# Kernel tuning notes

Hardware: AMD Instinct MI355X
Metric: run time of the kernel (lower is better)

The kernel has to match this reference:

```python
import jax, jax.numpy as jnp
import numpy as np

DIM = 1024
NUM_HEADS = 16
HEAD_DIM = DIM // NUM_HEADS
SCALE = HEAD_DIM ** (-0.5)
B, N = 2, 2048


def setup_inputs() -> dict:
    key = jax.random.key(0)
    ks = jax.random.split(key, 9)
    s = DIM ** (-0.5)
    return {
        "x": jax.random.normal(ks[0], (B, N, DIM), dtype=jnp.float32),
        "Wq": jax.random.normal(ks[1], (DIM, DIM), dtype=jnp.float32) * s,
        "bq": jax.random.normal(ks[2], (DIM,), dtype=jnp.float32) * 0.01,
        "Wk": jax.random.normal(ks[3], (DIM, DIM), dtype=jnp.float32) * s,
        "bk": jax.random.normal(ks[4], (DIM,), dtype=jnp.float32) * 0.01,
        "Wv": jax.random.normal(ks[5], (DIM, DIM), dtype=jnp.float32) * s,
        "bv": jax.random.normal(ks[6], (DIM,), dtype=jnp.float32) * 0.01,
        "Wp": jax.random.normal(ks[7], (DIM, DIM), dtype=jnp.float32) * s,
        "bp": jax.random.normal(ks[8], (DIM,), dtype=jnp.float32) * 0.01,
    }


def reference(x, Wq, bq, Wk, bk, Wv, bv, Wp, bp):
    Bb, Nn, C = x.shape
    # Linear layers (torch Linear: x @ W.T + b)
    q = x @ Wq.T + bq
    k = x @ Wk.T + bk
    v = x @ Wv.T + bv
    # [B, H, N, Dh]
    q = q.reshape(Bb, Nn, NUM_HEADS, HEAD_DIM).transpose(0, 2, 1, 3) * SCALE
    k = k.reshape(Bb, Nn, NUM_HEADS, HEAD_DIM).transpose(0, 2, 1, 3)
    v = v.reshape(Bb, Nn, NUM_HEADS, HEAD_DIM).transpose(0, 2, 1, 3)
    # float32 scores (original casts q,k to float before matmul)
    attn = jnp.einsum("bhnd,bhmd->bhnm", q.astype(jnp.float32), k.astype(jnp.float32))
    attn = jax.nn.softmax(attn, axis=-1).astype(x.dtype)
    out = jnp.einsum("bhnm,bhmd->bhnd", attn, v)
    out = out.transpose(0, 2, 1, 3).reshape(Bb, Nn, C)
    return out @ Wp.T + bp
```

## Files before the change

kernel.cpp:

```cpp
#include <hip/hip_runtime.h>
#include <hip/hip_bf16.h>
#include <stdint.h>

#define SEQ   2048
#define NDIM  1024
#define NH    16
#define DH    64
#define NB    2
#define MROWS (NB*SEQ)
#define ATTN_SCALE 0.125f

typedef __attribute__((ext_vector_type(8))) short bf16x8;
typedef __attribute__((ext_vector_type(4))) float f32x4;


__device__ __forceinline__ unsigned short f2bf(float f) {
  union { float f; unsigned int u; } v; v.f = f;
  unsigned int u = v.u;
  return (unsigned short)((u + 0x7fffu + ((u >> 16) & 1u)) >> 16);
}

__device__ __forceinline__ void gld16(const void* g, void* l) {
  __builtin_amdgcn_global_load_lds(
      (const __attribute__((address_space(1))) void*)g,
      (__attribute__((address_space(3))) void*)l,
      16, 0, 0);
}

__global__ __launch_bounds__(256) void cvt_all(
    const float* __restrict__ x,  const float* __restrict__ wq,
    const float* __restrict__ wk, const float* __restrict__ wv,
    const float* __restrict__ wp,
    unsigned short* __restrict__ xb,  unsigned short* __restrict__ wqb,
    unsigned short* __restrict__ wkb, unsigned short* __restrict__ wvb,
    unsigned short* __restrict__ wpb)
{
  int c = blockIdx.x * 256 + threadIdx.x;
  const float* s; unsigned short* d;
  if (c < (MROWS*NDIM/8)) { s = x; d = xb; }
  else {
    c -= MROWS*NDIM/8;
    int w = c >> 17; c &= (1<<17)-1;
    s = (w==0)?wq:(w==1)?wk:(w==2)?wv:wp;
    d = (w==0)?wqb:(w==1)?wkb:(w==2)?wvb:wpb;
  }
  size_t off = (size_t)c * 8;
  const float4* sp = (const float4*)(s + off);
  float4 a = sp[0], b4 = sp[1];
  unsigned int u0 = (unsigned)f2bf(a.x)  | ((unsigned)f2bf(a.y)  << 16);
  unsigned int u1 = (unsigned)f2bf(a.z)  | ((unsigned)f2bf(a.w)  << 16);
  unsigned int u2 = (unsigned)f2bf(b4.x) | ((unsigned)f2bf(b4.y) << 16);
  unsigned int u3 = (unsigned)f2bf(b4.z) | ((unsigned)f2bf(b4.w) << 16);
  uint4 o; o.x = u0; o.y = u1; o.z = u2; o.w = u3;
  *(uint4*)(d + off) = o;
}

__device__ __forceinline__ void gemm128_loop(
    const unsigned short* __restrict__ A0,
    const unsigned short* __restrict__ B0,
    int K, f32x4 acc[4][4], char* ldsA, char* ldsB)
{
  const int tid = threadIdx.x;
  const int lane = tid & 63;
  const int g    = lane >> 4;
  const int l15  = lane & 15;
  const int wv   = tid >> 6;
  const int wm   = wv >> 1;
  const int wn   = wv & 1;

  int srow[2], scol[2];
#pragma unroll
  for (int p = 0; p < 2; ++p) {
    int idx = p*256 + tid;
    int row = idx >> 2, cpos = idx & 3;
    srow[p] = row;
    scol[p] = (cpos ^ ((row >> 1) & 3)) * 8;
  }
  int offA[4], offB[4];
#pragma unroll
  for (int f = 0; f < 4; ++f) {
    int ra = wm*64 + f*16 + l15;
    offA[f] = ra*64 + ((g ^ ((ra >> 1) & 3)) * 16);
    int rb = wn*64 + f*16 + l15;
    offB[f] = rb*64 + ((g ^ ((rb >> 1) & 3)) * 16);
  }

  for (int k0 = 0; k0 < K; k0 += 32) {
#pragma unroll
    for (int p = 0; p < 2; ++p) {
      gld16(A0 + (size_t)srow[p]*K + k0 + scol[p], ldsA + p*4096 + wv*1024);
      gld16(B0 + (size_t)srow[p]*K + k0 + scol[p], ldsB + p*4096 + wv*1024);
    }
    __syncthreads();
    bf16x8 af[4], bfr[4];
#pragma unroll
    for (int f = 0; f < 4; ++f) {
      af[f]  = *(const bf16x8*)(ldsA + offA[f]);
      bfr[f] = *(const bf16x8*)(ldsB + offB[f]);
    }
#pragma unroll
    for (int i = 0; i < 4; ++i)
#pragma unroll
      for (int j = 0; j < 4; ++j)
        acc[i][j] = __builtin_amdgcn_mfma_f32_16x16x32_bf16(af[i], bfr[j], acc[i][j], 0, 0, 0);
    __syncthreads();
  }
}

__global__ __launch_bounds__(256, 3) void gemm_qkv(
    const unsigned short* __restrict__ xb,
    const unsigned short* __restrict__ wqb, const unsigned short* __restrict__ wkb,
    const unsigned short* __restrict__ wvb,
    const float* __restrict__ bq, const float* __restrict__ bk, const float* __restrict__ bv,
    unsigned short* __restrict__ qb, unsigned short* __restrict__ kb,
    unsigned short* __restrict__ vtb)
{
  __shared__ __align__(16) char lds[16384];
  const int z = blockIdx.z;
  const unsigned short* W = (z==0)?wqb:(z==1)?wkb:wvb;
  const float* bias = (z==0)?bq:(z==1)?bk:bv;
  const int n0 = blockIdx.x * 128, m0 = blockIdx.y * 128;

  f32x4 acc[4][4];
#pragma unroll
  for (int i = 0; i < 4; ++i)
#pragma unroll
    for (int j = 0; j < 4; ++j) acc[i][j] = (f32x4){0.f, 0.f, 0.f, 0.f};

  gemm128_loop(xb + (size_t)m0*NDIM, W + (size_t)n0*NDIM, NDIM, acc, lds, lds + 8192);

  const int lane = threadIdx.x & 63, g = lane >> 4, l15 = lane & 15;
  const int wvx = threadIdx.x >> 6, wm = wvx >> 1, wn = wvx & 1;

  if (z < 2) {
    unsigned short* out = (z==0) ? qb : kb;
#pragma unroll
    for (int i = 0; i < 4; ++i)
#pragma unroll
      for (int j = 0; j < 4; ++j) {
        int col = n0 + wn*64 + j*16 + l15;
        float bb = bias[col];
#pragma unroll
        for (int r = 0; r < 4; ++r) {
          int row = m0 + wm*64 + i*16 + g*4 + r;
          out[(size_t)row*NDIM + col] = f2bf(acc[i][j][r] + bb);
        }
      }
  } else {
#pragma unroll
    for (int i = 0; i < 4; ++i)
#pragma unroll
      for (int j = 0; j < 4; ++j) {
        int col = n0 + wn*64 + j*16 + l15;
        float bb = bias[col];
        int row0 = m0 + wm*64 + i*16 + g*4;
        int b_ = row0 >> 11, n_ = row0 & (SEQ-1);
        unsigned long long pk =
            (unsigned long long)f2bf(acc[i][j][0] + bb)
          | ((unsigned long long)f2bf(acc[i][j][1] + bb) << 16)
          | ((unsigned long long)f2bf(acc[i][j][2] + bb) << 32)
          | ((unsigned long long)f2bf(acc[i][j][3] + bb) << 48);
        *(unsigned long long*)(vtb + ((size_t)(b_*NDIM + col))*SEQ + n_) = pk;
      }
  }
}

__global__ __launch_bounds__(256, 2) void attn_fwd(
    const unsigned short* __restrict__ qb, const unsigned short* __restrict__ kb,
    const unsigned short* __restrict__ vtb, unsigned short* __restrict__ ob)
{
  __shared__ __align__(16) char lds[32768];
  char* Ks = lds;
  char* Vs = lds + 8192;
  const int tid = threadIdx.x, lane = tid & 63, g = lane >> 4, l15 = lane & 15;
  const int wvx = tid >> 6;
  char* Pw = lds + 16384 + wvx*4096;
  const int bh = blockIdx.y, b_ = bh >> 4, h = bh & 15;
  const int qbase = blockIdx.x*128 + wvx*32;

  bf16x8 qf[2][2];
#pragma unroll
  for (int fn = 0; fn < 2; ++fn)
#pragma unroll
    for (int kc = 0; kc < 2; ++kc) {
      size_t row = (size_t)(b_*SEQ + qbase + fn*16 + l15);
      qf[fn][kc] = *(const bf16x8*)(qb + row*NDIM + h*DH + kc*32 + g*8);
    }

  float m_[2] = {-3.0e38f, -3.0e38f};
  float l_[2] = {0.f, 0.f};
  f32x4 o_[2][4];
#pragma unroll
  for (int fn = 0; fn < 2; ++fn)
#pragma unroll
    for (int fd = 0; fd < 4; ++fd) o_[fn][fd] = (f32x4){0.f, 0.f, 0.f, 0.f};

  for (int t = 0; t < SEQ/64; ++t) {
    const int k0t = t*64;
#pragma unroll
    for (int p = 0; p < 2; ++p) {
      int idx = p*256 + tid;
      int row = idx >> 3, cpos = idx & 7;
      int gc8 = (cpos ^ (row & 7)) * 8;
      gld16(kb  + ((size_t)(b_*SEQ + k0t + row))*NDIM + h*DH + gc8,
            Ks + p*4096 + wvx*1024);
      gld16(vtb + ((size_t)(b_*NDIM + h*DH + row))*SEQ + k0t + gc8,
            Vs + p*4096 + wvx*1024);
    }
    __syncthreads();

    bf16x8 kf[4][2];
#pragma unroll
    for (int fm = 0; fm < 4; ++fm)
#pragma unroll
      for (int kc = 0; kc < 2; ++kc) {
        int row = fm*16 + l15;
        kf[fm][kc] = *(const bf16x8*)(Ks + row*128 + (((kc*4+g) ^ (row & 7))*16));
      }

    f32x4 st[2][4];
#pragma unroll
    for (int fn = 0; fn < 2; ++fn)
#pragma unroll
      for (int fm = 0; fm < 4; ++fm) st[fn][fm] = (f32x4){0.f, 0.f, 0.f, 0.f};
#pragma unroll
    for (int kc = 0; kc < 2; ++kc)
#pragma unroll
      for (int fn = 0; fn < 2; ++fn)
#pragma unroll
        for (int fm = 0; fm < 4; ++fm)
          st[fn][fm] = __builtin_amdgcn_mfma_f32_16x16x32_bf16(kf[fm][kc], qf[fn][kc], st[fn][fm], 0, 0, 0);

#pragma unroll
    for (int fn = 0; fn < 2; ++fn) {
      float xs[4][4];
      float tmax = -3.0e38f;
#pragma unroll
      for (int fm = 0; fm < 4; ++fm)
#pragma unroll
        for (int r = 0; r < 4; ++r) {
          float v = st[fn][fm][r] * ATTN_SCALE;
          xs[fm][r] = v;
          tmax = fmaxf(tmax, v);
        }
      tmax = fmaxf(tmax, __shfl_xor(tmax, 16));
      tmax = fmaxf(tmax, __shfl_xor(tmax, 32));
      float mnew  = fmaxf(m_[fn], tmax);
      float alpha = __expf(m_[fn] - mnew);
      m_[fn] = mnew;
      float rsum = 0.f;
      const int prow = fn*16 + l15;
#pragma unroll
      for (int fm = 0; fm < 4; ++fm) {
        float p0 = __expf(xs[fm][0] - mnew);
        float p1 = __expf(xs[fm][1] - mnew);
        float p2 = __expf(xs[fm][2] - mnew);
        float p3 = __expf(xs[fm][3] - mnew);
        rsum += (p0 + p1) + (p2 + p3);
        unsigned long long pk =
            (unsigned long long)f2bf(p0)
          | ((unsigned long long)f2bf(p1) << 16)
          | ((unsigned long long)f2bf(p2) << 32)
          | ((unsigned long long)f2bf(p3) << 48);
        *(unsigned long long*)(Pw + prow*128 + (((fm*2 + (g>>1)) ^ (prow & 7))*16) + (g & 1)*8) = pk;
      }
      rsum += __shfl_xor(rsum, 16);
      rsum += __shfl_xor(rsum, 32);
      l_[fn] = l_[fn]*alpha + rsum;
#pragma unroll
      for (int fd = 0; fd < 4; ++fd)
#pragma unroll
        for (int r = 0; r < 4; ++r) o_[fn][fd][r] *= alpha;
    }

    bf16x8 vf[4][2];
#pragma unroll
    for (int fd = 0; fd < 4; ++fd)
#pragma unroll
      for (int ks = 0; ks < 2; ++ks) {
        int row = fd*16 + l15;
        vf[fd][ks] = *(const bf16x8*)(Vs + row*128 + (((ks*4+g) ^ (row & 7))*16));
      }
    bf16x8 pf[2][2];
#pragma unroll
    for (int fn = 0; fn < 2; ++fn)
#pragma unroll
      for (int ks = 0; ks < 2; ++ks) {
        int row = fn*16 + l15;
        pf[fn][ks] = *(const bf16x8*)(Pw + row*128 + (((ks*4+g) ^ (row & 7))*16));
      }
#pragma unroll
    for (int ks = 0; ks < 2; ++ks)
#pragma unroll
      for (int fn = 0; fn < 2; ++fn)
#pragma unroll
        for (int fd = 0; fd < 4; ++fd)
          o_[fn][fd] = __builtin_amdgcn_mfma_f32_16x16x32_bf16(vf[fd][ks], pf[fn][ks], o_[fn][fd], 0, 0, 0);

    __syncthreads();
  }

#pragma unroll
  for (int fn = 0; fn < 2; ++fn) {
    float inv = 1.f / l_[fn];
    size_t row = (size_t)(b_*SEQ + qbase + fn*16 + l15);
#pragma unroll
    for (int fd = 0; fd < 4; ++fd) {
      unsigned long long pk =
          (unsigned long long)f2bf(o_[fn][fd][0]*inv)
        | ((unsigned long long)f2bf(o_[fn][fd][1]*inv) << 16)
        | ((unsigned long long)f2bf(o_[fn][fd][2]*inv) << 32)
        | ((unsigned long long)f2bf(o_[fn][fd][3]*inv) << 48);
      *(unsigned long long*)(ob + row*NDIM + h*DH + fd*16 + g*4) = pk;
    }
  }
}

__global__ __launch_bounds__(256, 3) void gemm_proj(
    const unsigned short* __restrict__ ob, const unsigned short* __restrict__ wpb,
    const float* __restrict__ bp, float* __restrict__ out)
{
  __shared__ __align__(16) char lds[16384];
  const int n0 = blockIdx.x * 128, m0 = blockIdx.y * 128;
  f32x4 acc[4][4];
#pragma unroll
  for (int i = 0; i < 4; ++i)
#pragma unroll
    for (int j = 0; j < 4; ++j) acc[i][j] = (f32x4){0.f, 0.f, 0.f, 0.f};

  gemm128_loop(ob + (size_t)m0*NDIM, wpb + (size_t)n0*NDIM, NDIM, acc, lds, lds + 8192);

  const int lane = threadIdx.x & 63, g = lane >> 4, l15 = lane & 15;
  const int wvx = threadIdx.x >> 6, wm = wvx >> 1, wn = wvx & 1;
#pragma unroll
  for (int i = 0; i < 4; ++i)
#pragma unroll
    for (int j = 0; j < 4; ++j) {
      int col = n0 + wn*64 + j*16 + l15;
      float bb = bp[col];
#pragma unroll
      for (int r = 0; r < 4; ++r) {
        int row = m0 + wm*64 + i*16 + g*4 + r;
        out[(size_t)row*NDIM + col] = acc[i][j][r] + bb;
      }
    }
}

extern "C" void kernel_launch(void* const* d_in, const int* in_sizes, int n_in,
                              void* d_out, int out_size, void* d_ws, size_t ws_size,
                              hipStream_t stream) {
  const float* x  = (const float*)d_in[0];
  const float* Wq = (const float*)d_in[1];
  const float* bq = (const float*)d_in[2];
  const float* Wk = (const float*)d_in[3];
  const float* bk = (const float*)d_in[4];
  const float* Wv = (const float*)d_in[5];
  const float* bv = (const float*)d_in[6];
  const float* Wp = (const float*)d_in[7];
  const float* bp = (const float*)d_in[8];
  float* out = (float*)d_out;

  char* ws = (char*)d_ws;
  const size_t MB = (size_t)1 << 20;
  unsigned short* xb  = (unsigned short*)(ws + 0*MB);
  unsigned short* wqb = (unsigned short*)(ws + 8*MB);
  unsigned short* wkb = (unsigned short*)(ws + 10*MB);
  unsigned short* wvb = (unsigned short*)(ws + 12*MB);
  unsigned short* wpb = (unsigned short*)(ws + 14*MB);
  unsigned short* qb  = (unsigned short*)(ws + 16*MB);
  unsigned short* kb  = (unsigned short*)(ws + 24*MB);
  unsigned short* vtb = (unsigned short*)(ws + 32*MB);
  unsigned short* ob  = (unsigned short*)(ws + 40*MB);

  hipLaunchKernelGGL(cvt_all, dim3(4096), dim3(256), 0, stream,
                     x, Wq, Wk, Wv, Wp, xb, wqb, wkb, wvb, wpb);
  hipLaunchKernelGGL(gemm_qkv, dim3(NDIM/128, MROWS/128, 3), dim3(256), 0, stream,
                     xb, wqb, wkb, wvb, bq, bk, bv, qb, kb, vtb);
  hipLaunchKernelGGL(attn_fwd, dim3(SEQ/128, NB*NH), dim3(256), 0, stream,
                     qb, kb, vtb, ob);
  hipLaunchKernelGGL(gemm_proj, dim3(NDIM/128, MROWS/128), dim3(256), 0, stream,
                     ob, wpb, bp, out);
}
```

Measured before the change: 216.0 us.

## Shrink attention and projection tiles for more blocks, use exp2 softmax with lazy rescale

The attention kernel now handles 64 query rows per block (16 per wave) instead of 128, with less LDS and a higher launch bound, which doubles the grid to fill more CUs. Softmax folds log2(e) into the scale, uses the hardware exp2 instruction, and skips the rescale of the accumulators when no row max increases. The output projection GEMM is templated to use 64-row M tiles, doubling its block count. In exchange, each K/V tile loaded into LDS is reused by fewer query rows, so K/V load traffic per output row goes up.

```diff
diff --git a/kernel.cpp b/kernel.cpp
--- a/kernel.cpp
+++ b/kernel.cpp
@@ -9,6 +9,7 @@
 #define NB    2
 #define MROWS (NB*SEQ)
 #define ATTN_SCALE 0.125f
+#define S2SCALE (0.125f * 1.44269504f)
 
 typedef __attribute__((ext_vector_type(8))) short bf16x8;
 typedef __attribute__((ext_vector_type(4))) float f32x4;
@@ -18,6 +19,14 @@
   union { float f; unsigned int u; } v; v.f = f;
   unsigned int u = v.u;
   return (unsigned short)((u + 0x7fffu + ((u >> 16) & 1u)) >> 16);
+}
+
+__device__ __forceinline__ float exp2fast(float x) {
+#if __has_builtin(__builtin_amdgcn_exp2f)
+  return __builtin_amdgcn_exp2f(x);
+#else
+  float r; asm volatile("v_exp_f32 %0, %1" : "=v"(r) : "v"(x)); return r;
+#endif
 }
 
 __device__ __forceinline__ void gld16(const void* g, void* l) {
@@ -55,11 +64,14 @@
   *(uint4*)(d + off) = o;
 }
 
-__device__ __forceinline__ void gemm128_loop(
+template<int BM>
+__device__ __forceinline__ void gemm_loop(
     const unsigned short* __restrict__ A0,
     const unsigned short* __restrict__ B0,
-    int K, f32x4 acc[4][4], char* ldsA, char* ldsB)
-{
+    int K, f32x4 (&acc)[BM/32][4], char* ldsA, char* ldsB)
+{
+  constexpr int MI = BM/32;
+  constexpr int AP = BM/64;
   const int tid = threadIdx.x;
   const int lane = tid & 63;
   const int g    = lane >> 4;
@@ -68,38 +80,48 @@
   const int wm   = wv >> 1;
   const int wn   = wv & 1;
 
-  int srow[2], scol[2];
+  int srowA[AP], scolA[AP], srowB[2], scolB[2];
+#pragma unroll
+  for (int p = 0; p < AP; ++p) {
+    int idx = p*256 + tid;
+    int row = idx >> 2, cpos = idx & 3;
+    srowA[p] = row;
+    scolA[p] = (cpos ^ ((row >> 1) & 3)) * 8;
+  }
 #pragma unroll
   for (int p = 0; p < 2; ++p) {
     int idx = p*256 + tid;
     int row = idx >> 2, cpos = idx & 3;
-    srow[p] = row;
-    scol[p] = (cpos ^ ((row >> 1) & 3)) * 8;
-  }
-  int offA[4], offB[4];
+    srowB[p] = row;
+    scolB[p] = (cpos ^ ((row >> 1) & 3)) * 8;
+  }
+  int offA[MI], offB[4];
+#pragma unroll
+  for (int f = 0; f < MI; ++f) {
+    int ra = wm*(BM/2) + f*16 + l15;
+    offA[f] = ra*64 + ((g ^ ((ra >> 1) & 3)) * 16);
+  }
 #pragma unroll
   for (int f = 0; f < 4; ++f) {
-    int ra = wm*64 + f*16 + l15;
-    offA[f] = ra*64 + ((g ^ ((ra >> 1) & 3)) * 16);
     int rb = wn*64 + f*16 + l15;
     offB[f] = rb*64 + ((g ^ ((rb >> 1) & 3)) * 16);
   }
 
   for (int k0 = 0; k0 < K; k0 += 32) {
 #pragma unroll
-    for (int p = 0; p < 2; ++p) {
-      gld16(A0 + (size_t)srow[p]*K + k0 + scol[p], ldsA + p*4096 + wv*1024);
-      gld16(B0 + (size_t)srow[p]*K + k0 + scol[p], ldsB + p*4096 + wv*1024);
-    }
+    for (int p = 0; p < AP; ++p)
+      gld16(A0 + (size_t)srowA[p]*K + k0 + scolA[p], ldsA + p*4096 + wv*1024);
+#pragma unroll
+    for (int p = 0; p < 2; ++p)
+      gld16(B0 + (size_t)srowB[p]*K + k0 + scolB[p], ldsB + p*4096 + wv*1024);
     __syncthreads();
-    bf16x8 af[4], bfr[4];
-#pragma unroll
-    for (int f = 0; f < 4; ++f) {
-      af[f]  = *(const bf16x8*)(ldsA + offA[f]);
-      bfr[f] = *(const bf16x8*)(ldsB + offB[f]);
-    }
-#pragma unroll
-    for (int i = 0; i < 4; ++i)
+    bf16x8 af[MI], bfr[4];
+#pragma unroll
+    for (int f = 0; f < MI; ++f) af[f] = *(const bf16x8*)(ldsA + offA[f]);
+#pragma unroll
+    for (int f = 0; f < 4;  ++f) bfr[f] = *(const bf16x8*)(ldsB + offB[f]);
+#pragma unroll
+    for (int i = 0; i < MI; ++i)
 #pragma unroll
       for (int j = 0; j < 4; ++j)
         acc[i][j] = __builtin_amdgcn_mfma_f32_16x16x32_bf16(af[i], bfr[j], acc[i][j], 0, 0, 0);
@@ -127,7 +149,7 @@
 #pragma unroll
     for (int j = 0; j < 4; ++j) acc[i][j] = (f32x4){0.f, 0.f, 0.f, 0.f};
 
-  gemm128_loop(xb + (size_t)m0*NDIM, W + (size_t)n0*NDIM, NDIM, acc, lds, lds + 8192);
+  gemm_loop<128>(xb + (size_t)m0*NDIM, W + (size_t)n0*NDIM, NDIM, acc, lds, lds + 8192);
 
   const int lane = threadIdx.x & 63, g = lane >> 4, l15 = lane & 15;
   const int wvx = threadIdx.x >> 6, wm = wvx >> 1, wn = wvx & 1;
@@ -165,35 +187,32 @@
   }
 }
 
-__global__ __launch_bounds__(256, 2) void attn_fwd(
+__global__ __launch_bounds__(256, 4) void attn_fwd(
     const unsigned short* __restrict__ qb, const unsigned short* __restrict__ kb,
     const unsigned short* __restrict__ vtb, unsigned short* __restrict__ ob)
 {
-  __shared__ __align__(16) char lds[32768];
+  __shared__ __align__(16) char lds[24576];
   char* Ks = lds;
   char* Vs = lds + 8192;
   const int tid = threadIdx.x, lane = tid & 63, g = lane >> 4, l15 = lane & 15;
   const int wvx = tid >> 6;
-  char* Pw = lds + 16384 + wvx*4096;
+  char* Pw = lds + 16384 + wvx*2048;
   const int bh = blockIdx.y, b_ = bh >> 4, h = bh & 15;
-  const int qbase = blockIdx.x*128 + wvx*32;
-
-  bf16x8 qf[2][2];
-#pragma unroll
-  for (int fn = 0; fn < 2; ++fn)
-#pragma unroll
-    for (int kc = 0; kc < 2; ++kc) {
-      size_t row = (size_t)(b_*SEQ + qbase + fn*16 + l15);
-      qf[fn][kc] = *(const bf16x8*)(qb + row*NDIM + h*DH + kc*32 + g*8);
-    }
-
-  float m_[2] = {-3.0e38f, -3.0e38f};
-  float l_[2] = {0.f, 0.f};
-  f32x4 o_[2][4];
-#pragma unroll
-  for (int fn = 0; fn < 2; ++fn)
-#pragma unroll
-    for (int fd = 0; fd < 4; ++fd) o_[fn][fd] = (f32x4){0.f, 0.f, 0.f, 0.f};
+  const int qbase = blockIdx.x*64 + wvx*16;
+
+  bf16x8 qf[2];
+  {
+    size_t row = (size_t)(b_*SEQ + qbase + l15);
+#pragma unroll
+    for (int kc = 0; kc < 2; ++kc)
+      qf[kc] = *(const bf16x8*)(qb + row*NDIM + h*DH + kc*32 + g*8);
+  }
+
+  float m2 = -3.0e38f;
+  float l_ = 0.f;
+  f32x4 o_[4];
+#pragma unroll
+  for (int fd = 0; fd < 4; ++fd) o_[fd] = (f32x4){0.f, 0.f, 0.f, 0.f};
 
   for (int t = 0; t < SEQ/64; ++t) {
     const int k0t = t*64;
@@ -218,60 +237,55 @@
         kf[fm][kc] = *(const bf16x8*)(Ks + row*128 + (((kc*4+g) ^ (row & 7))*16));
       }
 
-    f32x4 st[2][4];
-#pragma unroll
-    for (int fn = 0; fn < 2; ++fn)
-#pragma unroll
-      for (int fm = 0; fm < 4; ++fm) st[fn][fm] = (f32x4){0.f, 0.f, 0.f, 0.f};
+    f32x4 st[4];
+#pragma unroll
+    for (int fm = 0; fm < 4; ++fm) st[fm] = (f32x4){0.f, 0.f, 0.f, 0.f};
 #pragma unroll
     for (int kc = 0; kc < 2; ++kc)
 #pragma unroll
-      for (int fn = 0; fn < 2; ++fn)
-#pragma unroll
-        for (int fm = 0; fm < 4; ++fm)
-          st[fn][fm] = __builtin_amdgcn_mfma_f32_16x16x32_bf16(kf[fm][kc], qf[fn][kc], st[fn][fm], 0, 0, 0);
-
-#pragma unroll
-    for (int fn = 0; fn < 2; ++fn) {
-      float xs[4][4];
-      float tmax = -3.0e38f;
-#pragma unroll
       for (int fm = 0; fm < 4; ++fm)
-#pragma unroll
-        for (int r = 0; r < 4; ++r) {
-          float v = st[fn][fm][r] * ATTN_SCALE;
-          xs[fm][r] = v;
-          tmax = fmaxf(tmax, v);
-        }
-      tmax = fmaxf(tmax, __shfl_xor(tmax, 16));
-      tmax = fmaxf(tmax, __shfl_xor(tmax, 32));
-      float mnew  = fmaxf(m_[fn], tmax);
-      float alpha = __expf(m_[fn] - mnew);
-      m_[fn] = mnew;
-      float rsum = 0.f;
-      const int prow = fn*16 + l15;
-#pragma unroll
-      for (int fm = 0; fm < 4; ++fm) {
-        float p0 = __expf(xs[fm][0] - mnew);
-        float p1 = __expf(xs[fm][1] - mnew);
-        float p2 = __expf(xs[fm][2] - mnew);
-        float p3 = __expf(xs[fm][3] - mnew);
-        rsum += (p0 + p1) + (p2 + p3);
-        unsigned long long pk =
-            (unsigned long long)f2bf(p0)
-          | ((unsigned long long)f2bf(p1) << 16)
-          | ((unsigned long long)f2bf(p2) << 32)
-          | ((unsigned long long)f2bf(p3) << 48);
-        *(unsigned long long*)(Pw + prow*128 + (((fm*2 + (g>>1)) ^ (prow & 7))*16) + (g & 1)*8) = pk;
-      }
-      rsum += __shfl_xor(rsum, 16);
-      rsum += __shfl_xor(rsum, 32);
-      l_[fn] = l_[fn]*alpha + rsum;
+        st[fm] = __builtin_amdgcn_mfma_f32_16x16x32_bf16(kf[fm][kc], qf[kc], st[fm], 0, 0, 0);
+
+    float xs[4][4];
+    float tmax = -3.0e38f;
+#pragma unroll
+    for (int fm = 0; fm < 4; ++fm)
+#pragma unroll
+      for (int r = 0; r < 4; ++r) {
+        float v = st[fm][r] * S2SCALE;
+        xs[fm][r] = v;
+        tmax = fmaxf(tmax, v);
+      }
+    tmax = fmaxf(tmax, __shfl_xor(tmax, 16));
+    tmax = fmaxf(tmax, __shfl_xor(tmax, 32));
+    if (__any(tmax > m2)) {
+      float mnew  = fmaxf(m2, tmax);
+      float alpha = exp2fast(m2 - mnew);
+      m2 = mnew;
+      l_ *= alpha;
 #pragma unroll
       for (int fd = 0; fd < 4; ++fd)
 #pragma unroll
-        for (int r = 0; r < 4; ++r) o_[fn][fd][r] *= alpha;
-    }
+        for (int r = 0; r < 4; ++r) o_[fd][r] *= alpha;
+    }
+    float rsum = 0.f;
+#pragma unroll
+    for (int fm = 0; fm < 4; ++fm) {
+      float p0 = exp2fast(xs[fm][0] - m2);
+      float p1 = exp2fast(xs[fm][1] - m2);
+      float p2 = exp2fast(xs[fm][2] - m2);
+      float p3 = exp2fast(xs[fm][3] - m2);
+      rsum += (p0 + p1) + (p2 + p3);
+      unsigned long long pk =
+          (unsigned long long)f2bf(p0)
+        | ((unsigned long long)f2bf(p1) << 16)
+        | ((unsigned long long)f2bf(p2) << 32)
+        | ((unsigned long long)f2bf(p3) << 48);
+      *(unsigned long long*)(Pw + l15*128 + (((fm*2 + (g>>1)) ^ (l15 & 7))*16) + (g & 1)*8) = pk;
+    }
+    rsum += __shfl_xor(rsum, 16);
+    rsum += __shfl_xor(rsum, 32);
+    l_ += rsum;
 
     bf16x8 vf[4][2];
 #pragma unroll
@@ -281,66 +295,59 @@
         int row = fd*16 + l15;
         vf[fd][ks] = *(const bf16x8*)(Vs + row*128 + (((ks*4+g) ^ (row & 7))*16));
       }
-    bf16x8 pf[2][2];
-#pragma unroll
-    for (int fn = 0; fn < 2; ++fn)
-#pragma unroll
-      for (int ks = 0; ks < 2; ++ks) {
-        int row = fn*16 + l15;
-        pf[fn][ks] = *(const bf16x8*)(Pw + row*128 + (((ks*4+g) ^ (row & 7))*16));
-      }
+    bf16x8 pf[2];
 #pragma unroll
     for (int ks = 0; ks < 2; ++ks)
-#pragma unroll
-      for (int fn = 0; fn < 2; ++fn)
-#pragma unroll
-        for (int fd = 0; fd < 4; ++fd)
-          o_[fn][fd] = __builtin_amdgcn_mfma_f32_16x16x32_bf16(vf[fd][ks], pf[fn][ks], o_[fn][fd], 0, 0, 0);
+      pf[ks] = *(const bf16x8*)(Pw + l15*128 + (((ks*4+g) ^ (l15 & 7))*16));
+#pragma unroll
+    for (int ks = 0; ks < 2; ++ks)
+#pragma unroll
+      for (int fd = 0; fd < 4; ++fd)
+        o_[fd] = __builtin_amdgcn_mfma_f32_16x16x32_bf16(vf[fd][ks], pf[ks], o_[fd], 0, 0, 0);
 
     __syncthreads();
   }
 
-#pragma unroll
-  for (int fn = 0; fn < 2; ++fn) {
-    float inv = 1.f / l_[fn];
-    size_t row = (size_t)(b_*SEQ + qbase + fn*16 + l15);
+  {
+    float inv = 1.f / l_;
+    size_t row = (size_t)(b_*SEQ + qbase + l15);
 #pragma unroll
     for (int fd = 0; fd < 4; ++fd) {
       unsigned long long pk =
-          (unsigned long long)f2bf(o_[fn][fd][0]*inv)
-        | ((unsigned long long)f2bf(o_[fn][fd][1]*inv) << 16)
-        | ((unsigned long long)f2bf(o_[fn][fd][2]*inv) << 32)
-        | ((unsigned long long)f2bf(o_[fn][fd][3]*inv) << 48);
+          (unsigned long long)f2bf(o_[fd][0]*inv)
+        | ((unsigned long long)f2bf(o_[fd][1]*inv) << 16)
+        | ((unsigned long long)f2bf(o_[fd][2]*inv) << 32)
+        | ((unsigned long long)f2bf(o_[fd][3]*inv) << 48);
       *(unsigned long long*)(ob + row*NDIM + h*DH + fd*16 + g*4) = pk;
     }
   }
 }
 
-__global__ __launch_bounds__(256, 3) void gemm_proj(
+__global__ __launch_bounds__(256, 2) void gemm_proj(
     const unsigned short* __restrict__ ob, const unsigned short* __restrict__ wpb,
     const float* __restrict__ bp, float* __restrict__ out)
 {
-  __shared__ __align__(16) char lds[16384];
-  const int n0 = blockIdx.x * 128, m0 = blockIdx.y * 128;
-  f32x4 acc[4][4];
-#pragma unroll
-  for (int i = 0; i < 4; ++i)
+  __shared__ __align__(16) char lds[12288];
+  const int n0 = blockIdx.x * 128, m0 = blockIdx.y * 64;
+  f32x4 acc[2][4];
+#pragma unroll
+  for (int i = 0; i < 2; ++i)
 #pragma unroll
     for (int j = 0; j < 4; ++j) acc[i][j] = (f32x4){0.f, 0.f, 0.f, 0.f};
 
-  gemm128_loop(ob + (size_t)m0*NDIM, wpb + (size_t)n0*NDIM, NDIM, acc, lds, lds + 8192);
+  gemm_loop<64>(ob + (size_t)m0*NDIM, wpb + (size_t)n0*NDIM, NDIM, acc, lds, lds + 4096);
 
   const int lane = threadIdx.x & 63, g = lane >> 4, l15 = lane & 15;
   const int wvx = threadIdx.x >> 6, wm = wvx >> 1, wn = wvx & 1;
 #pragma unroll
-  for (int i = 0; i < 4; ++i)
+  for (int i = 0; i < 2; ++i)
 #pragma unroll
     for (int j = 0; j < 4; ++j) {
       int col = n0 + wn*64 + j*16 + l15;
       float bb = bp[col];
 #pragma unroll
       for (int r = 0; r < 4; ++r) {
-        int row = m0 + wm*64 + i*16 + g*4 + r;
+        int row = m0 + wm*32 + i*16 + g*4 + r;
         out[(size_t)row*NDIM + col] = acc[i][j][r] + bb;
       }
     }
@@ -376,8 +383,8 @@
                      x, Wq, Wk, Wv, Wp, xb, wqb, wkb, wvb, wpb);
   hipLaunchKernelGGL(gemm_qkv, dim3(NDIM/128, MROWS/128, 3), dim3(256), 0, stream,
                      xb, wqb, wkb, wvb, bq, bk, bv, qb, kb, vtb);
-  hipLaunchKernelGGL(attn_fwd, dim3(SEQ/128, NB*NH), dim3(256), 0, stream,
+  hipLaunchKernelGGL(attn_fwd, dim3(SEQ/64, NB*NH), dim3(256), 0, stream,
                      qb, kb, vtb, ob);
-  hipLaunchKernelGGL(gemm_proj, dim3(NDIM/128, MROWS/128), dim3(256), 0, stream,
+  hipLaunchKernelGGL(gemm_proj, dim3(NDIM/128, MROWS/64), dim3(256), 0, stream,
                      ob, wpb, bp, out);
 }
```

Result: faster. 210.1 us (-2.7%).
